# Performance work log

Measured on AMD Instinct MI355X. Metric: run time of the kernel, lower is better.

The kernel has to match this reference:

```python
import jax, jax.numpy as jnp
import numpy as np

B, T, H, F = 64, 512, 512, 32
G = 4 * H  # PyTorch LSTM gate stack: i, f, g, o


def setup_inputs() -> dict:
    key = jax.random.key(0)
    ks = jax.random.split(key, 20)
    s = 1.0 / np.sqrt(H)  # PyTorch LSTM/Linear init scale

    def w(k, shape):
        return (jax.random.normal(k, shape, jnp.float32) * s).astype(jnp.float32)

    inp = {"x": jax.random.normal(ks[0], (B, T, F), jnp.float32)}
    shapes = {
        "enc_Wih0": (G, F), "enc_Whh0": (G, H), "enc_bih0": (G,), "enc_bhh0": (G,),
        "enc_Wih1": (G, H), "enc_Whh1": (G, H), "enc_bih1": (G,), "enc_bhh1": (G,),
        "dec_Wih0": (G, F), "dec_Whh0": (G, H), "dec_bih0": (G,), "dec_bhh0": (G,),
        "dec_Wih1": (G, H), "dec_Whh1": (G, H), "dec_bih1": (G,), "dec_bhh1": (G,),
        "W_out": (F, H), "b_out": (F,),
    }
    for i, (name, shp) in enumerate(shapes.items()):
        inp[name] = w(ks[i + 1], shp)
    return inp


def _cell(x, h, c, Wih, Whh, bih, bhh):
    gates = x @ Wih.T + h @ Whh.T + bih + bhh  # [B, 4H]
    i, f, g, o = jnp.split(gates, 4, axis=-1)
    c2 = jax.nn.sigmoid(f) * c + jax.nn.sigmoid(i) * jnp.tanh(g)
    h2 = jax.nn.sigmoid(o) * jnp.tanh(c2)
    return h2, c2


def _layer(xs, Wih, Whh, bih, bhh):
    # xs: [T, B, in]; zero initial state as in nn.LSTM default
    h0 = jnp.zeros((xs.shape[1], Whh.shape[1]), xs.dtype)

    def step(carry, xt):
        h, c = carry
        h2, c2 = _cell(xt, h, c, Wih, Whh, bih, bhh)
        return (h2, c2), h2

    (hT, cT), ys = jax.lax.scan(step, (h0, h0), xs)
    return ys, hT, cT


def _forward(x, eW0, eU0, eb0, ec0, eW1, eU1, eb1, ec1,
             dW0, dU0, db0, dc0, dW1, dU1, db1, dc1, Wo, bo):
    xs = jnp.transpose(x, (1, 0, 2))  # time-major [T, B, F]
    # 2-layer encoder (dropout=0 in eval-style deterministic reference)
    ys0, h0, c0 = _layer(xs, eW0, eU0, eb0, ec0)
    _, h1, c1 = _layer(ys0, eW1, eU1, eb1, ec1)

    # Decoder replays inputs in reversed time order (teacher forcing branch).
    # Output at step i uses dec_hidden[0][0,:] == layer-0 hidden BEFORE the step.
    def step(carry, xt):
        hA, cA, hB, cB = carry
        out = hA @ Wo.T + bo  # hidden2out on decoder layer-0 hidden (faithful to source)
        hA2, cA2 = _cell(xt, hA, cA, dW0, dU0, db0, dc0)
        hB2, cB2 = _cell(hA2, hB, cB, dW1, dU1, db1, dc1)
        return (hA2, cA2, hB2, cB2), out

    _, outs = jax.lax.scan(step, (h0, c0, h1, c1), xs[::-1])
    return jnp.transpose(outs[::-1], (1, 0, 2))  # back to [B, T, F]


def reference(x, enc_Wih0, enc_Whh0, enc_bih0, enc_bhh0, enc_Wih1, enc_Whh1, enc_bih1, enc_bhh1, dec_Wih0, dec_Whh0, dec_bih0, dec_bhh0, dec_Wih1, dec_Whh1, dec_bih1, dec_bhh1, W_out, b_out):
    return _forward(x, enc_Wih0, enc_Whh0, enc_bih0, enc_bhh0,
                    enc_Wih1, enc_Whh1, enc_bih1, enc_bhh1,
                    dec_Wih0, dec_Whh0, dec_bih0, dec_bhh0,
                    dec_Wih1, dec_Whh1, dec_bih1, dec_bhh1, W_out, b_out)
```

## Files before the change

### kernel.cpp

```cpp
#include <hip/hip_runtime.h>


#define TT   512
#define HH   512
#define FF   32
#define KP   548
#define PODS 16
#define BT   4
#define JT   16
#define NTHR 256
#define NBLK 512
#define GRS  68
#define GPL  (BT * GRS + 8)
#define GRF  (16 * GPL)
#define U_FLOATS  (BT * KP)
#define OP3F 16
#define LDS_FLOATS (U_FLOATS + 2 * GRF + 3 * OP3F)
#define PUB_U32  (2 * PODS * BT * HH)

typedef float f4v __attribute__((ext_vector_type(4)));
typedef float f2v __attribute__((ext_vector_type(2)));
typedef unsigned long long u64;
typedef unsigned int u32;

__device__ __forceinline__ float sigmf(float x)    { return 1.f / (1.f + __expf(-x)); }
__device__ __forceinline__ float tanhfast(float x) { return 1.f - 2.f / (__expf(2.f * x) + 1.f); }

__device__ __forceinline__ void load_w(
    const float* __restrict__ Wih, const float* __restrict__ Whh,
    const float* __restrict__ bih, const float* __restrict__ bhh,
    int j0, int w, int kap, int gt,
    f2v wa01[4][4], f2v wa23[4][4], f2v wb01[4][4], f2v wb23[4][4],
    f2v wxv[4], float bias[4])
{
  #pragma unroll
  for (int m = 0; m < 4; ++m) {
    const int g = m * HH + j0 + gt;
    #pragma unroll
    for (int q = 0; q < 4; ++q) {
      const float* p = &Whh[g * HH + w * 128 + q * 32 + kap * 8];
      const f4v t0 = *(const f4v*)(p);
      const f4v t1 = *(const f4v*)(p + 4);
      f2v a; a[0] = t0[0]; a[1] = t0[1]; wa01[m][q] = a;
      f2v b; b[0] = t0[2]; b[1] = t0[3]; wa23[m][q] = b;
      f2v c; c[0] = t1[0]; c[1] = t1[1]; wb01[m][q] = c;
      f2v d; d[0] = t1[2]; d[1] = t1[3]; wb23[m][q] = d;
    }
    wxv[m]  = *(const f2v*)&Wih[g * FF + w * 8 + kap * 2];
    bias[m] = bih[g] + bhh[g];
  }
}

__global__ void init_ws_kernel(u32* pub) {
  const int i = blockIdx.x * blockDim.x + threadIdx.x;
  if (i < PUB_U32) pub[i] = 0u;
}

#define LDU64(P) __hip_atomic_load((P), __ATOMIC_RELAXED, __HIP_MEMORY_SCOPE_AGENT)

#define ISSUE(Q, GP) v[Q] = LDU64((const u64*)((GP) + 32 * (Q)))

#define WAITCH(Q) do {                                                         \
    unsigned lo_ = (unsigned)v[Q], hi_ = (unsigned)(v[Q] >> 32);               \
    int tries = 0;                                                             \
    while ((lo_ & 255u) != tg || (hi_ & 255u) != tg) {                         \
      if (++tries > 2) __builtin_amdgcn_s_sleep(1);                            \
      v[Q] = LDU64((const u64*)(gp + 32 * (Q)));                               \
      lo_ = (unsigned)v[Q]; hi_ = (unsigned)(v[Q] >> 32);                      \
    }                                                                          \
    float2 st_;                                                                \
    st_.x = __uint_as_float(lo_ & ~255u);                                      \
    st_.y = __uint_as_float(hi_ & ~255u);                                      \
    *(float2*)&Us[32 * (Q)] = st_;                                             \
  } while (0)

#define FMACHUNK(Q) do {                                                       \
    asm volatile("" ::: "memory");                                             \
    _Pragma("unroll")                                                          \
    for (int b = 0; b < 4; ++b) {                                              \
      const float* p = &U[b * KP + w * 128 + 32 * (Q) + 8 * kap];              \
      const f4v u0 = *(const f4v*)(p);                                         \
      const f4v u1 = *(const f4v*)(p + 4);                                     \
      f2v u0a; u0a[0] = u0[0]; u0a[1] = u0[1];                                 \
      f2v u0b; u0b[0] = u0[2]; u0b[1] = u0[3];                                 \
      f2v u1a; u1a[0] = u1[0]; u1a[1] = u1[1];                                 \
      f2v u1b; u1b[0] = u1[2]; u1b[1] = u1[3];                                 \
      _Pragma("unroll")                                                        \
      for (int m = 0; m < 4; ++m)                                              \
        acc2[m][b] += u0a * wa01[m][Q] + u0b * wa23[m][Q]                      \
                    + u1a * wb01[m][Q] + u1b * wb23[m][Q];                     \
    }                                                                          \
  } while (0)

__global__ void __launch_bounds__(NTHR, 2)
lstm_ae_kernel(const float* __restrict__ x,
               const float* __restrict__ eWih, const float* __restrict__ eWhh,
               const float* __restrict__ ebih, const float* __restrict__ ebhh,
               const float* __restrict__ dWih, const float* __restrict__ dWhh,
               const float* __restrict__ dbih, const float* __restrict__ dbhh,
               const float* __restrict__ Wo,  const float* __restrict__ bo,
               float* __restrict__ out, u32* __restrict__ pub)
{
  __shared__ float lds[LDS_FLOATS];
  float* U   = lds;
  float* Gr  = lds + U_FLOATS;
  float* OP3 = lds + U_FLOATS + 2 * GRF;

  const int tid = threadIdx.x;
  const int blk = blockIdx.x;
  const int pod = blk & (PODS - 1);
  const int gb  = blk >> 4;
  const int b0  = pod * BT;
  const int j0  = gb * JT;

  const int w    = tid >> 6;
  const int lane = tid & 63;
  const int row  = lane >> 4;
  const int sub  = lane & 15;

  const int kap = lane >> 4;
  const int gt  = lane & 15;

  const bool upd = tid < BT * JT;
  const int  ub  = tid >> 4, ujl = tid & 15;
  float c_reg = 0.f;

  f2v wa01[4][4], wa23[4][4], wb01[4][4], wb23[4][4], wxv[4];
  float bias[4];
  load_w(eWih, eWhh, ebih, ebhh, j0, w, kap, gt, wa01, wa23, wb01, wb23, wxv, bias);

  u64 v[4];
  {
    const u32* gp0 = pub + (size_t)pod * (BT * HH) + row * HH + 128 * w + 2 * sub;
    ISSUE(0, gp0); ISSUE(1, gp0);
  }

  #pragma unroll 1
  for (int phase = 0; phase < 2; ++phase) {
    #pragma unroll 1
    for (int step = 0; step < TT; ++step) {
      const int s = phase * TT + step;
      const unsigned tg = (unsigned)(s & 255);
      const int t = phase ? (TT - 1 - step) : step;
      const u32* prd = pub + (size_t)((s & 1) * PODS + pod) * (BT * HH);
      u32*       pwr = pub + (size_t)(((s + 1) & 1) * PODS + pod) * (BT * HH);
      float* Grp = Gr + (s & 1) * GRF;

      if (sub < 8)
        U[row * KP + HH + w * 8 + sub] =
            x[((size_t)(b0 + row) * TT + t) * FF + w * 8 + sub];

      f2v acc2[4][4];
      #pragma unroll
      for (int m = 0; m < 4; ++m)
        #pragma unroll
        for (int b = 0; b < 4; ++b) {
          f2v z; z[0] = ((w | kap) == 0) ? bias[m] : 0.f; z[1] = 0.f;
          acc2[m][b] = z;
        }

      const u32* gp = prd + row * HH + 128 * w + 2 * sub;
      float*     Us = U + row * KP + 128 * w + 2 * sub;

      WAITCH(0); ISSUE(2, gp); FMACHUNK(0);
      WAITCH(1); ISSUE(3, gp); FMACHUNK(1);
      WAITCH(2); FMACHUNK(2);
      WAITCH(3); FMACHUNK(3);

      #pragma unroll
      for (int b = 0; b < 4; ++b) {
        const f2v ux = *(const f2v*)&U[b * KP + HH + w * 8 + 2 * kap];
        #pragma unroll
        for (int m = 0; m < 4; ++m)
          acc2[m][b] += ux * wxv[m];
      }
      {
        float* Gw = Grp + (w * 4 + kap) * GPL + gt * 4;
        #pragma unroll
        for (int b = 0; b < 4; ++b) {
          f4v r;
          #pragma unroll
          for (int m = 0; m < 4; ++m) r[m] = acc2[m][b][0] + acc2[m][b][1];
          *(f4v*)&Gw[b * GRS] = r;
        }
      }
      __syncthreads();

      if (upd) {
        const float* g0 = Grp + ub * GRS + ujl * 4;
        float si = 0.f, sf = 0.f, sg = 0.f, so = 0.f;
        #pragma unroll
        for (int q = 0; q < 16; ++q) {
          const f4v g = *(const f4v*)(g0 + q * GPL);
          si += g[0]; sf += g[1]; sg += g[2]; so += g[3];
        }
        const float c2 = sigmf(sf) * c_reg + sigmf(si) * tanhfast(sg);
        const float h2 = sigmf(so) * tanhfast(c2);
        c_reg = c2;
        const unsigned pk = (__float_as_uint(h2) & ~255u)
                          | ((unsigned)(s + 1) & 255u);
        __hip_atomic_store(&pwr[ub * HH + j0 + ujl], pk,
                           __ATOMIC_RELAXED, __HIP_MEMORY_SCOPE_AGENT);
      }

      if (phase) {
        const float* wrow = Wo + gb * HH + w * 128 + sub * 8;
        const float* urow = U + row * KP + w * 128 + sub * 8;
        const f4v u0 = *(const f4v*)(urow);
        const f4v u1 = *(const f4v*)(urow + 4);
        const f4v q0 = *(const f4v*)(wrow);
        const f4v q1 = *(const f4v*)(wrow + 4);
        float pj = u0[0]*q0[0] + u0[1]*q0[1] + u0[2]*q0[2] + u0[3]*q0[3]
                 + u1[0]*q1[0] + u1[1]*q1[1] + u1[2]*q1[2] + u1[3]*q1[3];
        pj += __shfl_xor(pj, 1);
        pj += __shfl_xor(pj, 2);
        pj += __shfl_xor(pj, 4);
        pj += __shfl_xor(pj, 8);
        if (sub == 0) OP3[(s % 3) * OP3F + w * 4 + row] = pj;
        if (step > 0 && tid >= 192 && tid < 196) {
          const int b = tid - 192;
          const float* op = OP3 + ((s - 1) % 3) * OP3F + b;
          const float sm = op[0] + op[4] + op[8] + op[12];
          out[((size_t)(b0 + b) * TT + (t + 1)) * FF + gb] = sm + bo[gb];
        }
      }

      {
        const u32* gpn = (const u32*)pwr + row * HH + 128 * w + 2 * sub;
        ISSUE(0, gpn); ISSUE(1, gpn);
        asm volatile("" ::: "memory");
      }
    }
    if (phase == 0)
      load_w(dWih, dWhh, dbih, dbhh, j0, w, kap, gt, wa01, wa23, wb01, wb23, wxv, bias);
  }

  __syncthreads();
  if (tid >= 192 && tid < 196) {
    const int b = tid - 192;
    const float* op = OP3 + ((2 * TT - 1) % 3) * OP3F + b;
    const float sm = op[0] + op[4] + op[8] + op[12];
    out[((size_t)(b0 + b) * TT + 0) * FF + gb] = sm + bo[gb];
  }
}

extern "C" void kernel_launch(void* const* d_in, const int* in_sizes, int n_in,
                              void* d_out, int out_size, void* d_ws, size_t ws_size,
                              hipStream_t stream) {
  const float* x    = (const float*)d_in[0];
  const float* eWih = (const float*)d_in[1];
  const float* eWhh = (const float*)d_in[2];
  const float* ebih = (const float*)d_in[3];
  const float* ebhh = (const float*)d_in[4];
  const float* dWih = (const float*)d_in[9];
  const float* dWhh = (const float*)d_in[10];
  const float* dbih = (const float*)d_in[11];
  const float* dbhh = (const float*)d_in[12];
  const float* Wo   = (const float*)d_in[17];
  const float* bo   = (const float*)d_in[18];
  float* out = (float*)d_out;

  u32* pubbuf = (u32*)d_ws;

  init_ws_kernel<<<dim3((PUB_U32 + NTHR - 1) / NTHR), dim3(NTHR), 0, stream>>>(pubbuf);
  lstm_ae_kernel<<<dim3(NBLK), dim3(NTHR), 0, stream>>>(
      x, eWih, eWhh, ebih, ebhh, dWih, dWhh, dbih, dbhh, Wo, bo,
      out, pubbuf);
}
```

Before: 4.819 ms.

## Halve hidden units per block and double block count with single gate buffer

Each block now owns 8 hidden units instead of 16, so 1024 blocks are launched with launch bounds raised to 4 blocks per CU. The per-thread weight slice shrinks to f4v rows, and the x input is read straight into registers instead of staged through LDS. The gate-reduction buffer is now single-buffered, which requires a second __syncthreads per step, and only the first 32 column groups compute the output projection. The goal is more parallelism per recurrent step and lower register use, at the cost of an extra barrier, twice as many blocks in the cross-block handshake, and a longer 32-way gate reduction.

```diff
diff --git a/kernel.cpp b/kernel.cpp
--- a/kernel.cpp
+++ b/kernel.cpp
@@ -7,19 +7,18 @@
 #define KP   548
 #define PODS 16
 #define BT   4
-#define JT   16
+#define JT   8
 #define NTHR 256
-#define NBLK 512
-#define GRS  68
+#define NBLK 1024
+#define GRS  36
 #define GPL  (BT * GRS + 8)
-#define GRF  (16 * GPL)
+#define GRF  (32 * GPL)
 #define U_FLOATS  (BT * KP)
 #define OP3F 16
-#define LDS_FLOATS (U_FLOATS + 2 * GRF + 3 * OP3F)
+#define LDS_FLOATS (U_FLOATS + GRF + 3 * OP3F)
 #define PUB_U32  (2 * PODS * BT * HH)
 
 typedef float f4v __attribute__((ext_vector_type(4)));
-typedef float f2v __attribute__((ext_vector_type(2)));
 typedef unsigned long long u64;
 typedef unsigned int u32;
 
@@ -29,24 +28,15 @@
 __device__ __forceinline__ void load_w(
     const float* __restrict__ Wih, const float* __restrict__ Whh,
     const float* __restrict__ bih, const float* __restrict__ bhh,
-    int j0, int w, int kap, int gt,
-    f2v wa01[4][4], f2v wa23[4][4], f2v wb01[4][4], f2v wb23[4][4],
-    f2v wxv[4], float bias[4])
+    int j0, int w, int kap, int gt, f4v wv[4][4], float wx[4], float bias[4])
 {
   #pragma unroll
   for (int m = 0; m < 4; ++m) {
     const int g = m * HH + j0 + gt;
     #pragma unroll
-    for (int q = 0; q < 4; ++q) {
-      const float* p = &Whh[g * HH + w * 128 + q * 32 + kap * 8];
-      const f4v t0 = *(const f4v*)(p);
-      const f4v t1 = *(const f4v*)(p + 4);
-      f2v a; a[0] = t0[0]; a[1] = t0[1]; wa01[m][q] = a;
-      f2v b; b[0] = t0[2]; b[1] = t0[3]; wa23[m][q] = b;
-      f2v c; c[0] = t1[0]; c[1] = t1[1]; wb01[m][q] = c;
-      f2v d; d[0] = t1[2]; d[1] = t1[3]; wb23[m][q] = d;
-    }
-    wxv[m]  = *(const f2v*)&Wih[g * FF + w * 8 + kap * 2];
+    for (int q = 0; q < 4; ++q)
+      wv[m][q] = *(const f4v*)&Whh[g * HH + w * 128 + q * 32 + kap * 4];
+    wx[m]   = Wih[g * FF + w * 8 + kap];
     bias[m] = bih[g] + bhh[g];
   }
 }
@@ -78,21 +68,15 @@
     asm volatile("" ::: "memory");                                             \
     _Pragma("unroll")                                                          \
     for (int b = 0; b < 4; ++b) {                                              \
-      const float* p = &U[b * KP + w * 128 + 32 * (Q) + 8 * kap];              \
-      const f4v u0 = *(const f4v*)(p);                                         \
-      const f4v u1 = *(const f4v*)(p + 4);                                     \
-      f2v u0a; u0a[0] = u0[0]; u0a[1] = u0[1];                                 \
-      f2v u0b; u0b[0] = u0[2]; u0b[1] = u0[3];                                 \
-      f2v u1a; u1a[0] = u1[0]; u1a[1] = u1[1];                                 \
-      f2v u1b; u1b[0] = u1[2]; u1b[1] = u1[3];                                 \
+      const f4v u = *(const f4v*)&U[b * KP + w * 128 + 32 * (Q) + 4 * kap];    \
       _Pragma("unroll")                                                        \
       for (int m = 0; m < 4; ++m)                                              \
-        acc2[m][b] += u0a * wa01[m][Q] + u0b * wa23[m][Q]                      \
-                    + u1a * wb01[m][Q] + u1b * wb23[m][Q];                     \
+        acc[m][b] += u[0] * wv[m][Q][0] + u[1] * wv[m][Q][1]                   \
+                   + u[2] * wv[m][Q][2] + u[3] * wv[m][Q][3];                  \
     }                                                                          \
   } while (0)
 
-__global__ void __launch_bounds__(NTHR, 2)
+__global__ void __launch_bounds__(NTHR, 4)
 lstm_ae_kernel(const float* __restrict__ x,
                const float* __restrict__ eWih, const float* __restrict__ eWhh,
                const float* __restrict__ ebih, const float* __restrict__ ebhh,
@@ -104,7 +88,7 @@
   __shared__ float lds[LDS_FLOATS];
   float* U   = lds;
   float* Gr  = lds + U_FLOATS;
-  float* OP3 = lds + U_FLOATS + 2 * GRF;
+  float* OP3 = lds + U_FLOATS + GRF;
 
   const int tid = threadIdx.x;
   const int blk = blockIdx.x;
@@ -118,16 +102,16 @@
   const int row  = lane >> 4;
   const int sub  = lane & 15;
 
-  const int kap = lane >> 4;
-  const int gt  = lane & 15;
+  const int kap = lane >> 3;
+  const int gt  = lane & 7;
 
   const bool upd = tid < BT * JT;
-  const int  ub  = tid >> 4, ujl = tid & 15;
+  const int  ub  = tid >> 3, ujl = tid & 7;
   float c_reg = 0.f;
 
-  f2v wa01[4][4], wa23[4][4], wb01[4][4], wb23[4][4], wxv[4];
-  float bias[4];
-  load_w(eWih, eWhh, ebih, ebhh, j0, w, kap, gt, wa01, wa23, wb01, wb23, wxv, bias);
+  f4v  wv[4][4];
+  float wx[4], bias[4];
+  load_w(eWih, eWhh, ebih, ebhh, j0, w, kap, gt, wv, wx, bias);
 
   u64 v[4];
   {
@@ -144,20 +128,18 @@
       const int t = phase ? (TT - 1 - step) : step;
       const u32* prd = pub + (size_t)((s & 1) * PODS + pod) * (BT * HH);
       u32*       pwr = pub + (size_t)(((s + 1) & 1) * PODS + pod) * (BT * HH);
-      float* Grp = Gr + (s & 1) * GRF;
-
-      if (sub < 8)
-        U[row * KP + HH + w * 8 + sub] =
-            x[((size_t)(b0 + row) * TT + t) * FF + w * 8 + sub];
-
-      f2v acc2[4][4];
+
+      float xr[4];
+      #pragma unroll
+      for (int b = 0; b < 4; ++b)
+        xr[b] = x[((size_t)(b0 + b) * TT + t) * FF + 8 * w + kap];
+
+      float acc[4][4];
       #pragma unroll
       for (int m = 0; m < 4; ++m)
         #pragma unroll
-        for (int b = 0; b < 4; ++b) {
-          f2v z; z[0] = ((w | kap) == 0) ? bias[m] : 0.f; z[1] = 0.f;
-          acc2[m][b] = z;
-        }
+        for (int b = 0; b < 4; ++b)
+          acc[m][b] = ((w | kap) == 0) ? bias[m] : 0.f;
 
       const u32* gp = prd + row * HH + 128 * w + 2 * sub;
       float*     Us = U + row * KP + 128 * w + 2 * sub;
@@ -168,29 +150,28 @@
       WAITCH(3); FMACHUNK(3);
 
       #pragma unroll
-      for (int b = 0; b < 4; ++b) {
-        const f2v ux = *(const f2v*)&U[b * KP + HH + w * 8 + 2 * kap];
+      for (int b = 0; b < 4; ++b)
         #pragma unroll
         for (int m = 0; m < 4; ++m)
-          acc2[m][b] += ux * wxv[m];
-      }
+          acc[m][b] += xr[b] * wx[m];
+
       {
-        float* Gw = Grp + (w * 4 + kap) * GPL + gt * 4;
+        float* Gw = Gr + (w * 8 + kap) * GPL + gt * 4;
         #pragma unroll
         for (int b = 0; b < 4; ++b) {
           f4v r;
           #pragma unroll
-          for (int m = 0; m < 4; ++m) r[m] = acc2[m][b][0] + acc2[m][b][1];
+          for (int m = 0; m < 4; ++m) r[m] = acc[m][b];
           *(f4v*)&Gw[b * GRS] = r;
         }
       }
       __syncthreads();
 
       if (upd) {
-        const float* g0 = Grp + ub * GRS + ujl * 4;
+        const float* g0 = Gr + ub * GRS + ujl * 4;
         float si = 0.f, sf = 0.f, sg = 0.f, so = 0.f;
         #pragma unroll
-        for (int q = 0; q < 16; ++q) {
+        for (int q = 0; q < 32; ++q) {
           const f4v g = *(const f4v*)(g0 + q * GPL);
           si += g[0]; sf += g[1]; sg += g[2]; so += g[3];
         }
@@ -203,7 +184,7 @@
                            __ATOMIC_RELAXED, __HIP_MEMORY_SCOPE_AGENT);
       }
 
-      if (phase) {
+      if (phase && gb < FF) {
         const float* wrow = Wo + gb * HH + w * 128 + sub * 8;
         const float* urow = U + row * KP + w * 128 + sub * 8;
         const f4v u0 = *(const f4v*)(urow);
@@ -230,13 +211,13 @@
         ISSUE(0, gpn); ISSUE(1, gpn);
         asm volatile("" ::: "memory");
       }
+      __syncthreads();
     }
     if (phase == 0)
-      load_w(dWih, dWhh, dbih, dbhh, j0, w, kap, gt, wa01, wa23, wb01, wb23, wxv, bias);
-  }
-
-  __syncthreads();
-  if (tid >= 192 && tid < 196) {
+      load_w(dWih, dWhh, dbih, dbhh, j0, w, kap, gt, wv, wx, bias);
+  }
+
+  if (gb < FF && tid >= 192 && tid < 196) {
     const int b = tid - 192;
     const float* op = OP3 + ((2 * TT - 1) % 3) * OP3F + b;
     const float sm = op[0] + op[4] + op[8] + op[12];
```

Measured after the change: 8.175 ms. +69.6%, slower.
